# Optimization experiments

Hardware: AMD Instinct MI355X
Metric: run time of the kernel (lower is better)

Reference implementation:

```python
import jax, jax.numpy as jnp
import numpy as np

EPS = 1e-5
NH, NS = 8, 4


def layer_norm(x, g, b):
    m = jnp.mean(x, axis=-1, keepdims=True)
    v = jnp.mean((x - m) ** 2, axis=-1, keepdims=True)
    return (x - m) * jax.lax.rsqrt(v + EPS) * g + b


def grid_sample_border(feat, grid):
    # feat: (B,C,H,W), grid: (B,P,S,2) with (x,y) in [-1,1]; bilinear,
    # padding_mode='border', align_corners=True (matches F.grid_sample).
    B, C, H, W = feat.shape
    gx = jnp.clip((grid[..., 0] + 1.0) * 0.5 * (W - 1), 0.0, W - 1.0)
    gy = jnp.clip((grid[..., 1] + 1.0) * 0.5 * (H - 1), 0.0, H - 1.0)
    x0 = jnp.floor(gx)
    y0 = jnp.floor(gy)
    wx = (gx - x0)[:, None]  # (B,1,P,S)
    wy = (gy - y0)[:, None]
    x0i = x0.astype(jnp.int32)
    y0i = y0.astype(jnp.int32)
    x1i = jnp.minimum(x0i + 1, W - 1)
    y1i = jnp.minimum(y0i + 1, H - 1)
    ff = feat.reshape(B, C, H * W)
    gather = jax.vmap(lambda f, i: f[:, i])  # per-batch gather -> (B,C,P,S)
    v00 = gather(ff, y0i * W + x0i)
    v01 = gather(ff, y0i * W + x1i)
    v10 = gather(ff, y1i * W + x0i)
    v11 = gather(ff, y1i * W + x1i)
    return (v00 * (1 - wx) * (1 - wy) + v01 * wx * (1 - wy)
            + v10 * (1 - wx) * wy + v11 * wx * wy)


def setup_inputs() -> dict:
    key = jax.random.key(0)
    ks = jax.random.split(key, 32)
    dim, base = 256, 64
    hd = dim // NH
    inp = {
        'x': jax.random.normal(ks[0], (4, 6, 1024, dim), jnp.float32),
        'ref': jax.random.uniform(ks[1], (4, 1024, 2), jnp.float32) * 2.0 - 1.0,
        'feat0': jax.random.normal(ks[2], (4, base, 128, 128), jnp.float32),
        'feat1': jax.random.normal(ks[3], (4, base * 2, 64, 64), jnp.float32),
        'feat2': jax.random.normal(ks[4], (4, base * 4, 32, 32), jnp.float32),
        'feat3': jax.random.normal(ks[5], (4, base * 8, 16, 16), jnp.float32),
        'feat4': jax.random.normal(ks[6], (4, dim, 16, 16), jnp.float32),
        'norm1_g': jnp.ones((dim,), jnp.float32),
        'norm1_b': jnp.zeros((dim,), jnp.float32),
        'aw_W': 0.02 * jax.random.normal(ks[7], (dim, NH * NS), jnp.float32),
        'aw_b': 0.02 * jax.random.normal(ks[8], (NH * NS,), jnp.float32),
        'so_W': 0.02 * jax.random.normal(ks[9], (dim, 2 * NH * NS), jnp.float32),
        'so_b': 0.1 * jax.random.normal(ks[10], (2 * NH * NS,), jnp.float32),
        'ep0_W': 0.02 * jax.random.normal(ks[11], (base, hd), jnp.float32),
        'ep0_b': jnp.zeros((hd,), jnp.float32),
        'ep1_W': 0.02 * jax.random.normal(ks[12], (base * 2, hd), jnp.float32),
        'ep1_b': jnp.zeros((hd,), jnp.float32),
        'ep2_W': 0.02 * jax.random.normal(ks[13], (base * 4, hd), jnp.float32),
        'ep2_b': jnp.zeros((hd,), jnp.float32),
        'ep3_W': 0.02 * jax.random.normal(ks[14], (base * 8, hd), jnp.float32),
        'ep3_b': jnp.zeros((hd,), jnp.float32),
        'ep4_W': 0.02 * jax.random.normal(ks[15], (dim, hd), jnp.float32),
        'ep4_b': jnp.zeros((hd,), jnp.float32),
        'norm2_g': jnp.ones((dim,), jnp.float32),
        'norm2_b': jnp.zeros((dim,), jnp.float32),
        'fc1_W': 0.02 * jax.random.normal(ks[16], (dim, 2 * dim), jnp.float32),
        'fc1_b': jnp.zeros((2 * dim,), jnp.float32),
        'fc2_W': 0.02 * jax.random.normal(ks[17], (2 * dim, dim), jnp.float32),
        'fc2_b': jnp.zeros((dim,), jnp.float32),
    }
    return inp


def reference(x, ref, feat0, feat1, feat2, feat3, feat4,
              norm1_g, norm1_b, aw_W, aw_b, so_W, so_b,
              ep0_W, ep0_b, ep1_W, ep1_b, ep2_W, ep2_b, ep3_W, ep3_b, ep4_W, ep4_b,
              norm2_g, norm2_b, fc1_W, fc1_b, fc2_W, fc2_b):
    x0_tok, xq = x[:, :1], x[:, 1:]
    b, l, p, c = xq.shape
    hd = c // NH
    residual = xq
    h = layer_norm(xq + x0_tok, norm1_g, norm1_b)
    weights = jax.nn.softmax((h @ aw_W + aw_b).reshape(b, l, p, NH, NS), axis=-1)
    offsets = jnp.tanh((h @ so_W + so_b).reshape(b, l, p, NH * NS, 2))
    pos = offsets + ref[:, None, :, None, :]  # (b,l,p,S,2)
    feats = [feat0, feat1, feat2, feat3, feat4]
    eps_ = [(ep0_W, ep0_b), (ep1_W, ep1_b), (ep2_W, ep2_b), (ep3_W, ep3_b), (ep4_W, ep4_b)]
    sampled = []
    for idx in range(l):
        s = grid_sample_border(feats[idx], pos[:, idx])  # (b,C,p,S)
        s = jnp.transpose(s, (0, 2, 3, 1))                # (b,p,S,C)
        Wp, bp = eps_[idx]
        sampled.append(s @ Wp + bp)                       # (b,p,S,hd)
    fs = jnp.stack(sampled, axis=1).reshape(b, l, p, NH, NS, hd)
    out = jnp.einsum('blphs,blphsd->blphd', weights, fs).reshape(b, l, p, c)
    xq2 = residual + out
    h2 = layer_norm(xq2, norm2_g, norm2_b)
    mlp = jax.nn.gelu(h2 @ fc1_W + fc1_b, approximate=False) @ fc2_W + fc2_b
    xq2 = xq2 + mlp
    return jnp.concatenate([x0_tok, xq2], axis=1)
```

## Files before the change

kernel.cpp:

```cpp
#include <hip/hip_runtime.h>
#include <math.h>

#define B_ 4
#define L_ 5
#define P_ 1024
#define C_ 256
#define TOK (B_ * L_ * P_)

#define PF0_S 0u
#define PF1_S 2097152u
#define PF2_S 2621440u
#define PF3_S 2752512u
#define PF4_S 2785280u
#define WTS_F 1409024u
#define POSS_F 2064384u
#define U_S   0u
#define H2_S  10485760u
#define WC_S  17694720u
#define W1T_S 17719296u
#define W2T_S 17850368u
#define BCAT_F 8990720u
#define EWT_S  17981824u

typedef short bf16x8 __attribute__((ext_vector_type(8)));
typedef float f32x4  __attribute__((ext_vector_type(4)));

__device__ __forceinline__ unsigned short f2bf(float f) {
  unsigned u = __float_as_uint(f);
  unsigned r = (u + 0x7fffu + ((u >> 16) & 1u)) >> 16;
  return (unsigned short)r;
}
__device__ __forceinline__ float bf2f(unsigned short u) {
  return __uint_as_float((unsigned)u << 16);
}

__global__ void prep_all(const float* __restrict__ x, float* __restrict__ out,
                         const float* __restrict__ f1W, const float* __restrict__ f2W,
                         const float* __restrict__ awW, const float* __restrict__ soW,
                         const float* __restrict__ awb, const float* __restrict__ sob,
                         const float* __restrict__ e0W, const float* __restrict__ e1W,
                         const float* __restrict__ e2W, const float* __restrict__ e3W,
                         const float* __restrict__ e4W,
                         unsigned short* __restrict__ W1T, unsigned short* __restrict__ W2T,
                         unsigned short* __restrict__ Wc, unsigned short* __restrict__ eWT,
                         float* __restrict__ bcat) {
  int i = blockIdx.x * 256 + threadIdx.x;
  if (i < 1048576) {
    int b = i >> 18;
    int r = i & 262143;
    size_t off = (size_t)b * 6 * P_ * C_ + r;
    out[off] = x[off];
    return;
  }
  i -= 1048576;
  if (i < 131072) {
    int n = i >> 8, k = i & 255;
    W1T[i] = f2bf(f1W[k * 512 + n]);
  } else if (i < 262144) {
    int j = i - 131072;
    int n = j >> 9, k = j & 511;
    W2T[j] = f2bf(f2W[k * 256 + n]);
  } else if (i < 286720) {
    int j = i - 262144;
    int n = j >> 8, k = j & 255;
    Wc[j] = f2bf(n < 32 ? awW[k * 32 + n] : soW[k * 64 + (n - 32)]);
  } else if (i < 325632) {
    int j = i - 286720;
    const float* eW; int Cl, base, jj;
    if (j < 2048)       { eW = e0W; Cl = 64;  base = 0;     jj = j; }
    else if (j < 6144)  { eW = e1W; Cl = 128; base = 2048;  jj = j - 2048; }
    else if (j < 14336) { eW = e2W; Cl = 256; base = 6144;  jj = j - 6144; }
    else if (j < 30720) { eW = e3W; Cl = 512; base = 14336; jj = j - 14336; }
    else                { eW = e4W; Cl = 256; base = 30720; jj = j - 30720; }
    int d = jj / Cl, c = jj & (Cl - 1);
    eWT[base + jj] = f2bf(eW[c * 32 + d]);
  } else if (i < 325728) {
    int j = i - 325632;
    bcat[j] = j < 32 ? awb[j] : sob[j - 32];
  }
}

__global__ __launch_bounds__(256) void proj_gemm(
    const float* __restrict__ f0, const float* __restrict__ f1,
    const float* __restrict__ f2, const float* __restrict__ f3,
    const float* __restrict__ f4,
    const unsigned short* __restrict__ eWT,
    unsigned short* __restrict__ pf) {
  constexpr int LDK = 72;
  __shared__ unsigned short Al[64 * LDK];
  __shared__ unsigned short Bl[32 * LDK];
  int blk = blockIdx.x, tid = threadIdx.x;

  const float* feat; int Cl, HW, lt; unsigned pfo, eo;
  if (blk < 1024)      { feat = f0; Cl = 64;  HW = 16384; pfo = PF0_S; eo = 0;     lt = blk; }
  else if (blk < 1280) { feat = f1; Cl = 128; HW = 4096;  pfo = PF1_S; eo = 2048;  lt = blk - 1024; }
  else if (blk < 1344) { feat = f2; Cl = 256; HW = 1024;  pfo = PF2_S; eo = 6144;  lt = blk - 1280; }
  else if (blk < 1360) { feat = f3; Cl = 512; HW = 256;   pfo = PF3_S; eo = 14336; lt = blk - 1344; }
  else                 { feat = f4; Cl = 256; HW = 256;   pfo = PF4_S; eo = 30720; lt = blk - 1360; }
  int tpb = HW >> 6;
  int b = lt / tpb;
  int hw0 = (lt - b * tpb) * 64;
  const float* fb = feat + (size_t)b * Cl * HW;

  int cl = tid & 63, quad = tid >> 6;
  int w = tid >> 6, lane = tid & 63, q = lane >> 4, ml = lane & 15;

  f32x4 acc0 = (f32x4){0.f, 0.f, 0.f, 0.f};
  f32x4 acc1 = (f32x4){0.f, 0.f, 0.f, 0.f};

  for (int k0 = 0; k0 < Cl; k0 += 64) {
    if (k0) __syncthreads();
    { int rr = tid >> 3, kc = (tid & 7) * 8;
      *(int4*)(Bl + rr * LDK + kc) = *(const int4*)(eWT + eo + (size_t)rr * Cl + k0 + kc); }
    const float* src = fb + (size_t)(k0 + cl) * HW + hw0 + quad * 16;
    float4 v0 = *(const float4*)(src);
    float4 v1 = *(const float4*)(src + 4);
    float4 v2 = *(const float4*)(src + 8);
    float4 v3 = *(const float4*)(src + 12);
    unsigned short* ac = Al + cl;
    int mb = quad * 16;
    ac[(mb + 0)  * LDK] = f2bf(v0.x); ac[(mb + 1)  * LDK] = f2bf(v0.y);
    ac[(mb + 2)  * LDK] = f2bf(v0.z); ac[(mb + 3)  * LDK] = f2bf(v0.w);
    ac[(mb + 4)  * LDK] = f2bf(v1.x); ac[(mb + 5)  * LDK] = f2bf(v1.y);
    ac[(mb + 6)  * LDK] = f2bf(v1.z); ac[(mb + 7)  * LDK] = f2bf(v1.w);
    ac[(mb + 8)  * LDK] = f2bf(v2.x); ac[(mb + 9)  * LDK] = f2bf(v2.y);
    ac[(mb + 10) * LDK] = f2bf(v2.z); ac[(mb + 11) * LDK] = f2bf(v2.w);
    ac[(mb + 12) * LDK] = f2bf(v3.x); ac[(mb + 13) * LDK] = f2bf(v3.y);
    ac[(mb + 14) * LDK] = f2bf(v3.z); ac[(mb + 15) * LDK] = f2bf(v3.w);
    __syncthreads();
    #pragma unroll
    for (int ks = 0; ks < 2; ks++) {
      bf16x8 af = *(const bf16x8*)(Al + (w * 16 + ml) * LDK + ks * 32 + q * 8);
      bf16x8 b0 = *(const bf16x8*)(Bl + ml * LDK + ks * 32 + q * 8);
      bf16x8 b1 = *(const bf16x8*)(Bl + (16 + ml) * LDK + ks * 32 + q * 8);
      acc0 = __builtin_amdgcn_mfma_f32_16x16x32_bf16(af, b0, acc0, 0, 0, 0);
      acc1 = __builtin_amdgcn_mfma_f32_16x16x32_bf16(af, b1, acc1, 0, 0, 0);
    }
  }

  #pragma unroll
  for (int nt = 0; nt < 2; nt++) {
    f32x4 a = nt ? acc1 : acc0;
    int d = nt * 16 + ml;
    #pragma unroll
    for (int rr = 0; rr < 4; rr++) {
      int m = w * 16 + q * 4 + rr;
      pf[pfo + ((size_t)b * HW + hw0 + m) * 32 + d] = f2bf(a[rr]);
    }
  }
}

__global__ __launch_bounds__(256) void attn_prep(
    const float* __restrict__ x, const float* __restrict__ ref,
    const float* __restrict__ n1g, const float* __restrict__ n1b,
    const unsigned short* __restrict__ Wc, const float* __restrict__ bcat,
    float* __restrict__ wts, float* __restrict__ poss) {
  constexpr int LDA = 264;
  __shared__ unsigned short Al[64 * LDA];
  __shared__ unsigned short Bl[96 * 72];
  __shared__ float gg[C_], bb[C_];
  int t0 = blockIdx.x * 64;
  int tid = threadIdx.x;

  gg[tid] = n1g[tid];
  bb[tid] = n1b[tid];
  __syncthreads();

  #pragma unroll
  for (int half = 0; half < 2; ++half) {
    int r = half * 32 + (tid >> 3);
    int c0 = (tid & 7) * 32;
    int t = t0 + r;
    int b = t / (L_ * P_);
    int rr_ = t - b * (L_ * P_);
    int l = rr_ >> 10, p = rr_ & 1023;
    const float* xq = x + (((size_t)b * 6 + (l + 1)) * P_ + p) * C_ + c0;
    const float* x0 = x + (((size_t)b * 6) * P_ + p) * C_ + c0;
    float v[32];
    float s = 0.f, s2 = 0.f;
    #pragma unroll
    for (int i = 0; i < 32; i += 4) {
      float4 a = *(const float4*)(xq + i);
      float4 z = *(const float4*)(x0 + i);
      v[i] = a.x + z.x; v[i + 1] = a.y + z.y; v[i + 2] = a.z + z.z; v[i + 3] = a.w + z.w;
      s += v[i] + v[i + 1] + v[i + 2] + v[i + 3];
      s2 += v[i] * v[i] + v[i + 1] * v[i + 1] + v[i + 2] * v[i + 2] + v[i + 3] * v[i + 3];
    }
    #pragma unroll
    for (int off = 1; off < 8; off <<= 1) {
      s += __shfl_xor(s, off);
      s2 += __shfl_xor(s2, off);
    }
    float mean = s * (1.0f / C_);
    float var = s2 * (1.0f / C_) - mean * mean;
    float rs = rsqrtf(var + 1e-5f);
    unsigned short* dst = Al + r * LDA + c0;
    #pragma unroll
    for (int i = 0; i < 32; ++i)
      dst[i] = f2bf((v[i] - mean) * rs * gg[c0 + i] + bb[c0 + i]);
  }

  f32x4 acc[6];
  #pragma unroll
  for (int i = 0; i < 6; ++i) acc[i] = (f32x4){0.f, 0.f, 0.f, 0.f};
  int w = tid >> 6, lane = tid & 63, q = lane >> 4, ml = lane & 15;

  for (int k0 = 0; k0 < 256; k0 += 64) {
    __syncthreads();
    #pragma unroll
    for (int i = 0; i < 3; ++i) {
      int idx = tid + 256 * i;
      int rw = idx >> 3, kc = (idx & 7) * 8;
      *(int4*)(Bl + rw * 72 + kc) = *(const int4*)(Wc + (size_t)rw * 256 + k0 + kc);
    }
    __syncthreads();
    #pragma unroll
    for (int ks = 0; ks < 2; ++ks) {
      bf16x8 af = *(const bf16x8*)(Al + (w * 16 + ml) * LDA + k0 + ks * 32 + q * 8);
      #pragma unroll
      for (int nt = 0; nt < 6; ++nt) {
        bf16x8 bf = *(const bf16x8*)(Bl + (nt * 16 + ml) * 72 + ks * 32 + q * 8);
        acc[nt] = __builtin_amdgcn_mfma_f32_16x16x32_bf16(af, bf, acc[nt], 0, 0, 0);
      }
    }
  }

  #pragma unroll
  for (int nt = 0; nt < 6; ++nt) {
    int n = nt * 16 + ml;
    float bv = bcat[n];
    f32x4 a = acc[nt];
    if (nt < 2) {
      #pragma unroll
      for (int rr = 0; rr < 4; ++rr) {
        float v = a[rr] + bv;
        float m1 = fmaxf(v, __shfl_xor(v, 1));
        float m = fmaxf(m1, __shfl_xor(m1, 2));
        float e = expf(v - m);
        float su = e + __shfl_xor(e, 1);
        su += __shfl_xor(su, 2);
        int t = t0 + w * 16 + q * 4 + rr;
        wts[(size_t)t * 32 + n] = e / su;
      }
    } else {
      int j = n - 32;
      #pragma unroll
      for (int rr = 0; rr < 4; ++rr) {
        float v = a[rr] + bv;
        int t = t0 + w * 16 + q * 4 + rr;
        int b = t / (L_ * P_);
        int p = t & 1023;
        poss[(size_t)t * 64 + j] = tanhf(v) + ref[((size_t)b * P_ + p) * 2 + (j & 1)];
      }
    }
  }
}

__global__ __launch_bounds__(256) void sample_ln2(
    const float* __restrict__ x, const unsigned short* __restrict__ pf,
    const float* __restrict__ wts, const float* __restrict__ poss,
    const float* __restrict__ e0b, const float* __restrict__ e1b,
    const float* __restrict__ e2b, const float* __restrict__ e3b,
    const float* __restrict__ e4b,
    const float* __restrict__ n2g, const float* __restrict__ n2b,
    float* __restrict__ out, unsigned short* __restrict__ h2) {
  __shared__ float coef[128];
  __shared__ int   hwid[128];
  __shared__ float ra[4], rb[4];
  int t = blockIdx.x;
  int b = t / (L_ * P_);
  int r = t - b * (L_ * P_);
  int l = r >> 10;
  int p = r & 1023;
  int tid = threadIdx.x;

  int Hl; unsigned pfo; const float* eb;
  if (l == 0)      { Hl = 128; pfo = PF0_S; eb = e0b; }
  else if (l == 1) { Hl = 64;  pfo = PF1_S; eb = e1b; }
  else if (l == 2) { Hl = 32;  pfo = PF2_S; eb = e2b; }
  else if (l == 3) { Hl = 16;  pfo = PF3_S; eb = e3b; }
  else             { Hl = 16;  pfo = PF4_S; eb = e4b; }

  if (tid < 32) {
    int s = tid;
    float aw = wts[(size_t)t * 32 + s];
    float px = poss[(size_t)t * 64 + s * 2 + 0];
    float py = poss[(size_t)t * 64 + s * 2 + 1];
    float Wm = (float)(Hl - 1);
    float gx = fminf(fmaxf((px + 1.0f) * 0.5f * Wm, 0.0f), Wm);
    float gy = fminf(fmaxf((py + 1.0f) * 0.5f * Wm, 0.0f), Wm);
    float x0f = floorf(gx), y0f = floorf(gy);
    int x0 = (int)x0f, y0 = (int)y0f;
    int x1 = min(x0 + 1, Hl - 1), y1 = min(y0 + 1, Hl - 1);
    float wx = gx - x0f, wy = gy - y0f;
    int base = s * 4;
    hwid[base + 0] = y0 * Hl + x0; coef[base + 0] = aw * (1.f - wx) * (1.f - wy);
    hwid[base + 1] = y0 * Hl + x1; coef[base + 1] = aw * wx * (1.f - wy);
    hwid[base + 2] = y1 * Hl + x0; coef[base + 2] = aw * (1.f - wx) * wy;
    hwid[base + 3] = y1 * Hl + x1; coef[base + 3] = aw * wx * wy;
  }
  __syncthreads();

  int h = tid >> 5, d = tid & 31;
  const unsigned short* pfb = pf + pfo + (size_t)b * (Hl * Hl) * 32;
  float acc = 0.f;
  #pragma unroll
  for (int k = 0; k < 16; ++k)
    acc += coef[h * 16 + k] * bf2f(pfb[(size_t)hwid[h * 16 + k] * 32 + d]);

  size_t o = (((size_t)b * 6 + l + 1) * P_ + p) * C_ + tid;
  float v = x[o] + acc + eb[d];
  out[o] = v;

  float sa = v, s2 = v * v;
  #pragma unroll
  for (int off = 32; off > 0; off >>= 1) {
    sa += __shfl_xor(sa, off);
    s2 += __shfl_xor(s2, off);
  }
  if ((tid & 63) == 0) { ra[tid >> 6] = sa; rb[tid >> 6] = s2; }
  __syncthreads();
  float s  = ra[0] + ra[1] + ra[2] + ra[3];
  float ss = rb[0] + rb[1] + rb[2] + rb[3];
  float mean = s * (1.0f / C_);
  float var = ss * (1.0f / C_) - mean * mean;
  float hh = (v - mean) * rsqrtf(var + 1e-5f) * n2g[tid] + n2b[tid];
  h2[(size_t)t * C_ + tid] = f2bf(hh);
}

template<int MODE>
__global__ __launch_bounds__(256) void gemm_bf16(
    const unsigned short* __restrict__ A, const unsigned short* __restrict__ Bt,
    const float* __restrict__ bias, unsigned short* __restrict__ outU,
    float* __restrict__ outF, int N, int K) {
  constexpr int LDK = 72;
  __shared__ unsigned short Al[64 * LDK];
  __shared__ unsigned short Bl[64 * LDK];
  int m0 = blockIdx.x * 64, n0 = blockIdx.y * 64;
  int tid = threadIdx.x;
  int w = tid >> 6, lane = tid & 63;
  int q = lane >> 4, ml = lane & 15;
  int lr = tid >> 3;
  int lk = (tid & 7) * 8;

  f32x4 acc[4];
  #pragma unroll
  for (int i = 0; i < 4; i++) acc[i] = (f32x4){0.f, 0.f, 0.f, 0.f};

  for (int k0 = 0; k0 < K; k0 += 64) {
    int4 a0 = *(const int4*)(A + (size_t)(m0 + lr) * K + k0 + lk);
    int4 a1 = *(const int4*)(A + (size_t)(m0 + 32 + lr) * K + k0 + lk);
    int4 b0 = *(const int4*)(Bt + (size_t)(n0 + lr) * K + k0 + lk);
    int4 b1 = *(const int4*)(Bt + (size_t)(n0 + 32 + lr) * K + k0 + lk);
    __syncthreads();
    *(int4*)(Al + lr * LDK + lk) = a0;
    *(int4*)(Al + (32 + lr) * LDK + lk) = a1;
    *(int4*)(Bl + lr * LDK + lk) = b0;
    *(int4*)(Bl + (32 + lr) * LDK + lk) = b1;
    __syncthreads();
    #pragma unroll
    for (int ks = 0; ks < 2; ks++) {
      bf16x8 af = *(const bf16x8*)(Al + (w * 16 + ml) * LDK + ks * 32 + q * 8);
      #pragma unroll
      for (int nt = 0; nt < 4; nt++) {
        bf16x8 bf = *(const bf16x8*)(Bl + (nt * 16 + ml) * LDK + ks * 32 + q * 8);
        acc[nt] = __builtin_amdgcn_mfma_f32_16x16x32_bf16(af, bf, acc[nt], 0, 0, 0);
      }
    }
  }

  #pragma unroll
  for (int nt = 0; nt < 4; nt++) {
    int n = n0 + nt * 16 + ml;
    float bv = bias[n];
    #pragma unroll
    for (int rr = 0; rr < 4; rr++) {
      int m = m0 + w * 16 + q * 4 + rr;
      float v = acc[nt][rr] + bv;
      if (MODE == 0) {
        v = 0.5f * v * (1.0f + erff(v * 0.70710678118654752f));
        outU[(size_t)m * N + n] = f2bf(v);
      } else {
        int s = m >> 10;
        int p = m & 1023;
        int bb = s / 5, ll = s - bb * 5;
        size_t o = (((size_t)bb * 6 + ll + 1) * P_ + p) * C_ + n;
        outF[o] += v;
      }
    }
  }
}

extern "C" void kernel_launch(void* const* d_in, const int* in_sizes, int n_in,
                              void* d_out, int out_size, void* d_ws, size_t ws_size,
                              hipStream_t stream) {
  const float* x     = (const float*)d_in[0];
  const float* ref   = (const float*)d_in[1];
  const float* feat0 = (const float*)d_in[2];
  const float* feat1 = (const float*)d_in[3];
  const float* feat2 = (const float*)d_in[4];
  const float* feat3 = (const float*)d_in[5];
  const float* feat4 = (const float*)d_in[6];
  const float* n1g   = (const float*)d_in[7];
  const float* n1b   = (const float*)d_in[8];
  const float* awW   = (const float*)d_in[9];
  const float* awb   = (const float*)d_in[10];
  const float* soW   = (const float*)d_in[11];
  const float* sob   = (const float*)d_in[12];
  const float* e0W   = (const float*)d_in[13];
  const float* e0b   = (const float*)d_in[14];
  const float* e1W   = (const float*)d_in[15];
  const float* e1b   = (const float*)d_in[16];
  const float* e2W   = (const float*)d_in[17];
  const float* e2b   = (const float*)d_in[18];
  const float* e3W   = (const float*)d_in[19];
  const float* e3b   = (const float*)d_in[20];
  const float* e4W   = (const float*)d_in[21];
  const float* e4b   = (const float*)d_in[22];
  const float* n2g   = (const float*)d_in[23];
  const float* n2b   = (const float*)d_in[24];
  const float* f1W   = (const float*)d_in[25];
  const float* f1b   = (const float*)d_in[26];
  const float* f2W   = (const float*)d_in[27];
  const float* f2b   = (const float*)d_in[28];

  float* wsf = (float*)d_ws;
  unsigned short* ws16 = (unsigned short*)d_ws;
  unsigned short* pf  = ws16;
  float* wts  = wsf + WTS_F;
  float* poss = wsf + POSS_F;
  unsigned short* u   = ws16 + U_S;
  unsigned short* h2  = ws16 + H2_S;
  unsigned short* Wc  = ws16 + WC_S;
  unsigned short* W1T = ws16 + W1T_S;
  unsigned short* W2T = ws16 + W2T_S;
  unsigned short* eWT = ws16 + EWT_S;
  float* bcat = wsf + BCAT_F;
  float* out = (float*)d_out;

  prep_all<<<5369, 256, 0, stream>>>(x, out, f1W, f2W, awW, soW, awb, sob,
                                     e0W, e1W, e2W, e3W, e4W,
                                     W1T, W2T, Wc, eWT, bcat);

  proj_gemm<<<1376, 256, 0, stream>>>(feat0, feat1, feat2, feat3, feat4, eWT, pf);

  attn_prep<<<320, 256, 0, stream>>>(x, ref, n1g, n1b, Wc, bcat, wts, poss);

  sample_ln2<<<TOK, 256, 0, stream>>>(x, pf, wts, poss,
                                      e0b, e1b, e2b, e3b, e4b,
                                      n2g, n2b, out, h2);

  gemm_bf16<0><<<dim3(320, 8), 256, 0, stream>>>(h2, W1T, f1b, u, nullptr, 512, 256);

  gemm_bf16<1><<<dim3(320, 4), 256, 0, stream>>>(u, W2T, f2b, nullptr, out, 256, 512);
}
```

Before: 238.1 us.

## Fuse MLP GEMMs, fold weight prep into consumers, two tokens per sampling block

Removes the separate prep kernel. Projection and attention weights are now converted to bf16 inside proj_gemm and attn_prep, and the copy plus MLP weight transposes run as extra blocks of attn_prep. The two MLP GEMMs become one fused kernel that keeps the GELU intermediate in shared memory and reads W2T straight from global memory. sample_ln2 now handles two tokens per block with paired bf16 loads. This cuts kernel launches and the round trip of the intermediate activation through memory, but fused_mlp runs only 320 blocks holding large accumulators, and weight conversion is repeated in every block.

Measured after the change: 339.6 us. 42.7% more time.

```diff
diff --git a/kernel.cpp b/kernel.cpp
--- a/kernel.cpp
+++ b/kernel.cpp
@@ -14,13 +14,9 @@
 #define PF4_S 2785280u
 #define WTS_F 1409024u
 #define POSS_F 2064384u
-#define U_S   0u
 #define H2_S  10485760u
-#define WC_S  17694720u
 #define W1T_S 17719296u
 #define W2T_S 17850368u
-#define BCAT_F 8990720u
-#define EWT_S  17981824u
 
 typedef short bf16x8 __attribute__((ext_vector_type(8)));
 typedef float f32x4  __attribute__((ext_vector_type(4)));
@@ -34,69 +30,25 @@
   return __uint_as_float((unsigned)u << 16);
 }
 
-__global__ void prep_all(const float* __restrict__ x, float* __restrict__ out,
-                         const float* __restrict__ f1W, const float* __restrict__ f2W,
-                         const float* __restrict__ awW, const float* __restrict__ soW,
-                         const float* __restrict__ awb, const float* __restrict__ sob,
-                         const float* __restrict__ e0W, const float* __restrict__ e1W,
-                         const float* __restrict__ e2W, const float* __restrict__ e3W,
-                         const float* __restrict__ e4W,
-                         unsigned short* __restrict__ W1T, unsigned short* __restrict__ W2T,
-                         unsigned short* __restrict__ Wc, unsigned short* __restrict__ eWT,
-                         float* __restrict__ bcat) {
-  int i = blockIdx.x * 256 + threadIdx.x;
-  if (i < 1048576) {
-    int b = i >> 18;
-    int r = i & 262143;
-    size_t off = (size_t)b * 6 * P_ * C_ + r;
-    out[off] = x[off];
-    return;
-  }
-  i -= 1048576;
-  if (i < 131072) {
-    int n = i >> 8, k = i & 255;
-    W1T[i] = f2bf(f1W[k * 512 + n]);
-  } else if (i < 262144) {
-    int j = i - 131072;
-    int n = j >> 9, k = j & 511;
-    W2T[j] = f2bf(f2W[k * 256 + n]);
-  } else if (i < 286720) {
-    int j = i - 262144;
-    int n = j >> 8, k = j & 255;
-    Wc[j] = f2bf(n < 32 ? awW[k * 32 + n] : soW[k * 64 + (n - 32)]);
-  } else if (i < 325632) {
-    int j = i - 286720;
-    const float* eW; int Cl, base, jj;
-    if (j < 2048)       { eW = e0W; Cl = 64;  base = 0;     jj = j; }
-    else if (j < 6144)  { eW = e1W; Cl = 128; base = 2048;  jj = j - 2048; }
-    else if (j < 14336) { eW = e2W; Cl = 256; base = 6144;  jj = j - 6144; }
-    else if (j < 30720) { eW = e3W; Cl = 512; base = 14336; jj = j - 14336; }
-    else                { eW = e4W; Cl = 256; base = 30720; jj = j - 30720; }
-    int d = jj / Cl, c = jj & (Cl - 1);
-    eWT[base + jj] = f2bf(eW[c * 32 + d]);
-  } else if (i < 325728) {
-    int j = i - 325632;
-    bcat[j] = j < 32 ? awb[j] : sob[j - 32];
-  }
-}
-
 __global__ __launch_bounds__(256) void proj_gemm(
     const float* __restrict__ f0, const float* __restrict__ f1,
     const float* __restrict__ f2, const float* __restrict__ f3,
     const float* __restrict__ f4,
-    const unsigned short* __restrict__ eWT,
+    const float* __restrict__ e0W, const float* __restrict__ e1W,
+    const float* __restrict__ e2W, const float* __restrict__ e3W,
+    const float* __restrict__ e4W,
     unsigned short* __restrict__ pf) {
   constexpr int LDK = 72;
   __shared__ unsigned short Al[64 * LDK];
   __shared__ unsigned short Bl[32 * LDK];
   int blk = blockIdx.x, tid = threadIdx.x;
 
-  const float* feat; int Cl, HW, lt; unsigned pfo, eo;
-  if (blk < 1024)      { feat = f0; Cl = 64;  HW = 16384; pfo = PF0_S; eo = 0;     lt = blk; }
-  else if (blk < 1280) { feat = f1; Cl = 128; HW = 4096;  pfo = PF1_S; eo = 2048;  lt = blk - 1024; }
-  else if (blk < 1344) { feat = f2; Cl = 256; HW = 1024;  pfo = PF2_S; eo = 6144;  lt = blk - 1280; }
-  else if (blk < 1360) { feat = f3; Cl = 512; HW = 256;   pfo = PF3_S; eo = 14336; lt = blk - 1344; }
-  else                 { feat = f4; Cl = 256; HW = 256;   pfo = PF4_S; eo = 30720; lt = blk - 1360; }
+  const float* feat; const float* eW; int Cl, HW, lt; unsigned pfo;
+  if (blk < 1024)      { feat = f0; eW = e0W; Cl = 64;  HW = 16384; pfo = PF0_S; lt = blk; }
+  else if (blk < 1280) { feat = f1; eW = e1W; Cl = 128; HW = 4096;  pfo = PF1_S; lt = blk - 1024; }
+  else if (blk < 1344) { feat = f2; eW = e2W; Cl = 256; HW = 1024;  pfo = PF2_S; lt = blk - 1280; }
+  else if (blk < 1360) { feat = f3; eW = e3W; Cl = 512; HW = 256;   pfo = PF3_S; lt = blk - 1344; }
+  else                 { feat = f4; eW = e4W; Cl = 256; HW = 256;   pfo = PF4_S; lt = blk - 1360; }
   int tpb = HW >> 6;
   int b = lt / tpb;
   int hw0 = (lt - b * tpb) * 64;
@@ -110,8 +62,12 @@
 
   for (int k0 = 0; k0 < Cl; k0 += 64) {
     if (k0) __syncthreads();
-    { int rr = tid >> 3, kc = (tid & 7) * 8;
-      *(int4*)(Bl + rr * LDK + kc) = *(const int4*)(eWT + eo + (size_t)rr * Cl + k0 + kc); }
+    #pragma unroll
+    for (int i = 0; i < 8; ++i) {
+      int idx = tid + 256 * i;
+      int d = idx >> 6, k = idx & 63;
+      Bl[d * LDK + k] = f2bf(eW[(size_t)(k0 + k) * 32 + d]);
+    }
     const float* src = fb + (size_t)(k0 + cl) * HW + hw0 + quad * 16;
     float4 v0 = *(const float4*)(src);
     float4 v1 = *(const float4*)(src + 4);
@@ -153,15 +109,41 @@
 __global__ __launch_bounds__(256) void attn_prep(
     const float* __restrict__ x, const float* __restrict__ ref,
     const float* __restrict__ n1g, const float* __restrict__ n1b,
-    const unsigned short* __restrict__ Wc, const float* __restrict__ bcat,
+    const float* __restrict__ awW, const float* __restrict__ soW,
+    const float* __restrict__ awb, const float* __restrict__ sob,
+    const float* __restrict__ f1W, const float* __restrict__ f2W,
+    float* __restrict__ out, unsigned short* __restrict__ W1T,
+    unsigned short* __restrict__ W2T,
     float* __restrict__ wts, float* __restrict__ poss) {
   constexpr int LDA = 264;
   __shared__ unsigned short Al[64 * LDA];
   __shared__ unsigned short Bl[96 * 72];
   __shared__ float gg[C_], bb[C_];
-  int t0 = blockIdx.x * 64;
+  int blk = blockIdx.x;
   int tid = threadIdx.x;
 
+  if (blk >= 320) {
+    int i = (blk - 320) * 256 + tid;
+    if (i < 1048576) {
+      int b = i >> 18;
+      int r = i & 262143;
+      size_t off = (size_t)b * 6 * P_ * C_ + r;
+      out[off] = x[off];
+    } else {
+      i -= 1048576;
+      if (i < 131072) {
+        int n = i >> 8, k = i & 255;
+        W1T[i] = f2bf(f1W[k * 512 + n]);
+      } else {
+        int j = i - 131072;
+        int n = j >> 9, k = j & 511;
+        W2T[j] = f2bf(f2W[k * 256 + n]);
+      }
+    }
+    return;
+  }
+
+  int t0 = blk * 64;
   gg[tid] = n1g[tid];
   bb[tid] = n1b[tid];
   __syncthreads();
@@ -208,10 +190,12 @@
   for (int k0 = 0; k0 < 256; k0 += 64) {
     __syncthreads();
     #pragma unroll
-    for (int i = 0; i < 3; ++i) {
+    for (int i = 0; i < 24; ++i) {
       int idx = tid + 256 * i;
-      int rw = idx >> 3, kc = (idx & 7) * 8;
-      *(int4*)(Bl + rw * 72 + kc) = *(const int4*)(Wc + (size_t)rw * 256 + k0 + kc);
+      int n = idx >> 6, k = idx & 63;
+      float wv = (n < 32) ? awW[(size_t)(k0 + k) * 32 + n]
+                          : soW[(size_t)(k0 + k) * 64 + (n - 32)];
+      Bl[n * 72 + k] = f2bf(wv);
     }
     __syncthreads();
     #pragma unroll
@@ -228,7 +212,7 @@
   #pragma unroll
   for (int nt = 0; nt < 6; ++nt) {
     int n = nt * 16 + ml;
-    float bv = bcat[n];
+    float bv = (n < 32) ? awb[n] : sob[n - 32];
     f32x4 a = acc[nt];
     if (nt < 2) {
       #pragma unroll
@@ -264,14 +248,13 @@
     const float* __restrict__ e4b,
     const float* __restrict__ n2g, const float* __restrict__ n2b,
     float* __restrict__ out, unsigned short* __restrict__ h2) {
-  __shared__ float coef[128];
-  __shared__ int   hwid[128];
+  __shared__ float coef[256];
+  __shared__ int   hwid[256];
   __shared__ float ra[4], rb[4];
-  int t = blockIdx.x;
-  int b = t / (L_ * P_);
-  int r = t - b * (L_ * P_);
-  int l = r >> 10;
-  int p = r & 1023;
+  int t0 = blockIdx.x * 2;
+  int b = t0 / (L_ * P_);
+  int r0 = t0 - b * (L_ * P_);
+  int l = r0 >> 10;
   int tid = threadIdx.x;
 
   int Hl; unsigned pfo; const float* eb;
@@ -281,8 +264,9 @@
   else if (l == 3) { Hl = 16;  pfo = PF3_S; eb = e3b; }
   else             { Hl = 16;  pfo = PF4_S; eb = e4b; }
 
-  if (tid < 32) {
-    int s = tid;
+  if (tid < 64) {
+    int tl = tid >> 5, s = tid & 31;
+    int t = t0 + tl;
     float aw = wts[(size_t)t * 32 + s];
     float px = poss[(size_t)t * 64 + s * 2 + 0];
     float py = poss[(size_t)t * 64 + s * 2 + 1];
@@ -293,7 +277,7 @@
     int x0 = (int)x0f, y0 = (int)y0f;
     int x1 = min(x0 + 1, Hl - 1), y1 = min(y0 + 1, Hl - 1);
     float wx = gx - x0f, wy = gy - y0f;
-    int base = s * 4;
+    int base = tid * 4;
     hwid[base + 0] = y0 * Hl + x0; coef[base + 0] = aw * (1.f - wx) * (1.f - wy);
     hwid[base + 1] = y0 * Hl + x1; coef[base + 1] = aw * wx * (1.f - wy);
     hwid[base + 2] = y1 * Hl + x0; coef[base + 2] = aw * (1.f - wx) * wy;
@@ -301,92 +285,132 @@
   }
   __syncthreads();
 
-  int h = tid >> 5, d = tid & 31;
+  int tl = tid >> 7;
+  int ch0 = (tid & 127) * 2;
+  int h = ch0 >> 5, d = ch0 & 31;
+  int t = t0 + tl;
+  int p = (r0 + tl) & 1023;
   const unsigned short* pfb = pf + pfo + (size_t)b * (Hl * Hl) * 32;
-  float acc = 0.f;
-  #pragma unroll
-  for (int k = 0; k < 16; ++k)
-    acc += coef[h * 16 + k] * bf2f(pfb[(size_t)hwid[h * 16 + k] * 32 + d]);
-
-  size_t o = (((size_t)b * 6 + l + 1) * P_ + p) * C_ + tid;
-  float v = x[o] + acc + eb[d];
-  out[o] = v;
-
-  float sa = v, s2 = v * v;
+  int cb = tl * 128 + h * 16;
+  float acc0 = 0.f, acc1 = 0.f;
+  #pragma unroll
+  for (int k = 0; k < 16; ++k) {
+    float cf = coef[cb + k];
+    unsigned uv = *(const unsigned*)(pfb + (size_t)hwid[cb + k] * 32 + d);
+    acc0 += cf * bf2f((unsigned short)(uv & 0xffffu));
+    acc1 += cf * bf2f((unsigned short)(uv >> 16));
+  }
+
+  size_t o = (((size_t)b * 6 + l + 1) * P_ + p) * C_ + ch0;
+  float2 xr = *(const float2*)(x + o);
+  float v0 = xr.x + acc0 + eb[d];
+  float v1 = xr.y + acc1 + eb[d + 1];
+  *(float2*)(out + o) = make_float2(v0, v1);
+
+  float sa = v0 + v1, s2 = v0 * v0 + v1 * v1;
   #pragma unroll
   for (int off = 32; off > 0; off >>= 1) {
     sa += __shfl_xor(sa, off);
     s2 += __shfl_xor(s2, off);
   }
-  if ((tid & 63) == 0) { ra[tid >> 6] = sa; rb[tid >> 6] = s2; }
+  int wv = tid >> 6;
+  if ((tid & 63) == 0) { ra[wv] = sa; rb[wv] = s2; }
   __syncthreads();
-  float s  = ra[0] + ra[1] + ra[2] + ra[3];
-  float ss = rb[0] + rb[1] + rb[2] + rb[3];
+  float s  = ra[tl * 2] + ra[tl * 2 + 1];
+  float ss = rb[tl * 2] + rb[tl * 2 + 1];
   float mean = s * (1.0f / C_);
   float var = ss * (1.0f / C_) - mean * mean;
-  float hh = (v - mean) * rsqrtf(var + 1e-5f) * n2g[tid] + n2b[tid];
-  h2[(size_t)t * C_ + tid] = f2bf(hh);
-}
-
-template<int MODE>
-__global__ __launch_bounds__(256) void gemm_bf16(
-    const unsigned short* __restrict__ A, const unsigned short* __restrict__ Bt,
-    const float* __restrict__ bias, unsigned short* __restrict__ outU,
-    float* __restrict__ outF, int N, int K) {
+  float rs = rsqrtf(var + 1e-5f);
+  unsigned short h0 = f2bf((v0 - mean) * rs * n2g[ch0] + n2b[ch0]);
+  unsigned short h1 = f2bf((v1 - mean) * rs * n2g[ch0 + 1] + n2b[ch0 + 1]);
+  *(unsigned*)(h2 + (size_t)t * C_ + ch0) = (unsigned)h0 | ((unsigned)h1 << 16);
+}
+
+__global__ __launch_bounds__(256) void fused_mlp(
+    const unsigned short* __restrict__ h2,
+    const unsigned short* __restrict__ W1T, const unsigned short* __restrict__ W2T,
+    const float* __restrict__ f1b, const float* __restrict__ f2b,
+    float* __restrict__ out) {
+  constexpr int LDA = 264;
   constexpr int LDK = 72;
-  __shared__ unsigned short Al[64 * LDK];
-  __shared__ unsigned short Bl[64 * LDK];
-  int m0 = blockIdx.x * 64, n0 = blockIdx.y * 64;
-  int tid = threadIdx.x;
-  int w = tid >> 6, lane = tid & 63;
-  int q = lane >> 4, ml = lane & 15;
-  int lr = tid >> 3;
-  int lk = (tid & 7) * 8;
-
-  f32x4 acc[4];
-  #pragma unroll
-  for (int i = 0; i < 4; i++) acc[i] = (f32x4){0.f, 0.f, 0.f, 0.f};
-
-  for (int k0 = 0; k0 < K; k0 += 64) {
-    int4 a0 = *(const int4*)(A + (size_t)(m0 + lr) * K + k0 + lk);
-    int4 a1 = *(const int4*)(A + (size_t)(m0 + 32 + lr) * K + k0 + lk);
-    int4 b0 = *(const int4*)(Bt + (size_t)(n0 + lr) * K + k0 + lk);
-    int4 b1 = *(const int4*)(Bt + (size_t)(n0 + 32 + lr) * K + k0 + lk);
+  __shared__ unsigned short Ah[64 * LDA];
+  __shared__ unsigned short Us[64 * LDK];
+  __shared__ unsigned short Bs[64 * LDK];
+  int m0 = blockIdx.x * 64, tid = threadIdx.x;
+  int w = tid >> 6, lane = tid & 63, q = lane >> 4, ml = lane & 15;
+
+  #pragma unroll
+  for (int i = 0; i < 8; ++i) {
+    int idx = tid + 256 * i;
+    int r = idx >> 5, c8 = (idx & 31) * 8;
+    *(int4*)(Ah + r * LDA + c8) = *(const int4*)(h2 + (size_t)(m0 + r) * 256 + c8);
+  }
+
+  f32x4 acc2[16];
+  #pragma unroll
+  for (int i = 0; i < 16; ++i) acc2[i] = (f32x4){0.f, 0.f, 0.f, 0.f};
+
+  for (int uc = 0; uc < 8; ++uc) {
+    f32x4 acc1[4];
+    #pragma unroll
+    for (int i = 0; i < 4; ++i) acc1[i] = (f32x4){0.f, 0.f, 0.f, 0.f};
+    for (int k0 = 0; k0 < 256; k0 += 64) {
+      __syncthreads();
+      #pragma unroll
+      for (int i = 0; i < 2; ++i) {
+        int idx = tid + 256 * i;
+        int rr = idx >> 3, kc = (idx & 7) * 8;
+        *(int4*)(Bs + rr * LDK + kc) =
+            *(const int4*)(W1T + (size_t)(uc * 64 + rr) * 256 + k0 + kc);
+      }
+      __syncthreads();
+      #pragma unroll
+      for (int ks = 0; ks < 2; ++ks) {
+        bf16x8 af = *(const bf16x8*)(Ah + (w * 16 + ml) * LDA + k0 + ks * 32 + q * 8);
+        #pragma unroll
+        for (int nt = 0; nt < 4; ++nt) {
+          bf16x8 bf = *(const bf16x8*)(Bs + (nt * 16 + ml) * LDK + ks * 32 + q * 8);
+          acc1[nt] = __builtin_amdgcn_mfma_f32_16x16x32_bf16(af, bf, acc1[nt], 0, 0, 0);
+        }
+      }
+    }
     __syncthreads();
-    *(int4*)(Al + lr * LDK + lk) = a0;
-    *(int4*)(Al + (32 + lr) * LDK + lk) = a1;
-    *(int4*)(Bl + lr * LDK + lk) = b0;
-    *(int4*)(Bl + (32 + lr) * LDK + lk) = b1;
+    #pragma unroll
+    for (int nt = 0; nt < 4; ++nt) {
+      int ucol = nt * 16 + ml;
+      float bv = f1b[uc * 64 + ucol];
+      #pragma unroll
+      for (int rr = 0; rr < 4; ++rr) {
+        float v = acc1[nt][rr] + bv;
+        v = 0.5f * v * (1.0f + erff(v * 0.70710678118654752f));
+        Us[(w * 16 + q * 4 + rr) * LDK + ucol] = f2bf(v);
+      }
+    }
     __syncthreads();
     #pragma unroll
-    for (int ks = 0; ks < 2; ks++) {
-      bf16x8 af = *(const bf16x8*)(Al + (w * 16 + ml) * LDK + ks * 32 + q * 8);
-      #pragma unroll
-      for (int nt = 0; nt < 4; nt++) {
-        bf16x8 bf = *(const bf16x8*)(Bl + (nt * 16 + ml) * LDK + ks * 32 + q * 8);
-        acc[nt] = __builtin_amdgcn_mfma_f32_16x16x32_bf16(af, bf, acc[nt], 0, 0, 0);
-      }
-    }
-  }
-
-  #pragma unroll
-  for (int nt = 0; nt < 4; nt++) {
-    int n = n0 + nt * 16 + ml;
-    float bv = bias[n];
-    #pragma unroll
-    for (int rr = 0; rr < 4; rr++) {
+    for (int ks = 0; ks < 2; ++ks) {
+      bf16x8 af = *(const bf16x8*)(Us + (w * 16 + ml) * LDK + ks * 32 + q * 8);
+      #pragma unroll
+      for (int nt = 0; nt < 16; ++nt) {
+        bf16x8 bf = *(const bf16x8*)(W2T + (size_t)(nt * 16 + ml) * 512 +
+                                     uc * 64 + ks * 32 + q * 8);
+        acc2[nt] = __builtin_amdgcn_mfma_f32_16x16x32_bf16(af, bf, acc2[nt], 0, 0, 0);
+      }
+    }
+  }
+
+  #pragma unroll
+  for (int nt = 0; nt < 16; ++nt) {
+    int n = nt * 16 + ml;
+    float bv = f2b[n];
+    #pragma unroll
+    for (int rr = 0; rr < 4; ++rr) {
       int m = m0 + w * 16 + q * 4 + rr;
-      float v = acc[nt][rr] + bv;
-      if (MODE == 0) {
-        v = 0.5f * v * (1.0f + erff(v * 0.70710678118654752f));
-        outU[(size_t)m * N + n] = f2bf(v);
-      } else {
-        int s = m >> 10;
-        int p = m & 1023;
-        int bb = s / 5, ll = s - bb * 5;
-        size_t o = (((size_t)bb * 6 + ll + 1) * P_ + p) * C_ + n;
-        outF[o] += v;
-      }
+      int s = m >> 10;
+      int p = m & 1023;
+      int bb = s / 5, ll = s - bb * 5;
+      size_t o = (((size_t)bb * 6 + ll + 1) * P_ + p) * C_ + n;
+      out[o] += acc2[nt][rr] + bv;
     }
   }
 }
@@ -429,28 +453,20 @@
   unsigned short* pf  = ws16;
   float* wts  = wsf + WTS_F;
   float* poss = wsf + POSS_F;
-  unsigned short* u   = ws16 + U_S;
   unsigned short* h2  = ws16 + H2_S;
-  unsigned short* Wc  = ws16 + WC_S;
   unsigned short* W1T = ws16 + W1T_S;
   unsigned short* W2T = ws16 + W2T_S;
-  unsigned short* eWT = ws16 + EWT_S;
-  float* bcat = wsf + BCAT_F;
   float* out = (float*)d_out;
 
-  prep_all<<<5369, 256, 0, stream>>>(x, out, f1W, f2W, awW, soW, awb, sob,
-                                     e0W, e1W, e2W, e3W, e4W,
-                                     W1T, W2T, Wc, eWT, bcat);
-
-  proj_gemm<<<1376, 256, 0, stream>>>(feat0, feat1, feat2, feat3, feat4, eWT, pf);
-
-  attn_prep<<<320, 256, 0, stream>>>(x, ref, n1g, n1b, Wc, bcat, wts, poss);
-
-  sample_ln2<<<TOK, 256, 0, stream>>>(x, pf, wts, poss,
-                                      e0b, e1b, e2b, e3b, e4b,
-                                      n2g, n2b, out, h2);
-
-  gemm_bf16<0><<<dim3(320, 8), 256, 0, stream>>>(h2, W1T, f1b, u, nullptr, 512, 256);
-
-  gemm_bf16<1><<<dim3(320, 4), 256, 0, stream>>>(u, W2T, f2b, nullptr, out, 256, 512);
-}
+  attn_prep<<<5440, 256, 0, stream>>>(x, ref, n1g, n1b, awW, soW, awb, sob,
+                                      f1W, f2W, out, W1T, W2T, wts, poss);
+
+  proj_gemm<<<1376, 256, 0, stream>>>(feat0, feat1, feat2, feat3, feat4,
+                                      e0W, e1W, e2W, e3W, e4W, pf);
+
+  sample_ln2<<<TOK / 2, 256, 0, stream>>>(x, pf, wts, poss,
+                                          e0b, e1b, e2b, e3b, e4b,
+                                          n2g, n2b, out, h2);
+
+  fused_mlp<<<320, 256, 0, stream>>>(h2, W1T, W2T, f1b, f2b, out);
+}
```
